# Kernel optimization log

Hardware: AMD Instinct MI355X
Metric: run time of the kernel (lower is better)

## Reference

```python
import jax, jax.numpy as jnp
import numpy as np

EMBED = 1024
HEADS = 16


def setup_inputs() -> dict:
    key = jax.random.key(0)
    k1, k2, k3 = jax.random.split(key, 3)
    B, S, D = 2, 2048, EMBED
    x = jax.random.normal(k1, (B, S, D), dtype=jnp.float32)
    # nn.Linear weights: stored as [out, in]; y = x @ W.T
    w_qkv = jax.random.normal(k2, (3 * D, D), dtype=jnp.float32) * (D ** -0.5)
    w_out = jax.random.normal(k3, (D, D), dtype=jnp.float32) * (D ** -0.5)
    return {"x": x, "w_qkv": w_qkv, "w_out": w_out}


def reference(x, w_qkv, w_out):
    B, S, D = x.shape
    H = HEADS
    hd = D // H
    qkv = x @ w_qkv.T                       # [B, S, 3D]
    q, k, v = jnp.split(qkv, 3, axis=-1)
    # 'b l (head k) -> b head l k'
    def heads(t):
        return t.reshape(B, S, H, hd).transpose(0, 2, 1, 3)
    q, k, v = heads(q), heads(k), heads(v)
    scale = hd ** 0.5
    scores = jnp.einsum('bhqd,bhkd->bhqk', q, k) / scale
    probs = jax.nn.softmax(scores, axis=-1)
    out = jnp.einsum('bhqk,bhkd->bhqd', probs, v)  # [B, H, S, hd]
    out = out.transpose(0, 2, 1, 3).reshape(B, S, D)
    return out @ w_out.T
```

## Files before the change

### kernel.cpp

```cpp
#include <hip/hip_runtime.h>

typedef short short8 __attribute__((ext_vector_type(8)));
typedef short short4v __attribute__((ext_vector_type(4)));
typedef float floatx4 __attribute__((ext_vector_type(4)));
typedef unsigned short ushort_t;

#define EMBED 1024
#define HEADS 16
#define HD 64
#define SEQ 2048
#define BATCH 2

__device__ inline ushort_t f2bf(float f) {
    unsigned int u = __float_as_uint(f);
    u += 0x7fff + ((u >> 16) & 1);
    return (ushort_t)(u >> 16);
}

typedef const __attribute__((address_space(1))) unsigned int* gas_t;
typedef __attribute__((address_space(3))) unsigned int* las_t;
__device__ inline void async_copy16(const ushort_t* g, ushort_t* l) {
    __builtin_amdgcn_global_load_lds((gas_t)g, (las_t)l, 16, 0, 0);
}

__global__ void cast3_kernel(const float* __restrict__ a, ushort_t* __restrict__ oa, int na,
                             const float* __restrict__ b, ushort_t* __restrict__ ob, int nb,
                             const float* __restrict__ c, ushort_t* __restrict__ oc, int nc) {
    int idx = (blockIdx.x * blockDim.x + threadIdx.x) * 4;
    const float* in; ushort_t* out;
    if (idx < na)            { in = a;  out = oa; }
    else if (idx < na + nb)  { in = b;  out = ob; idx -= na; }
    else if (idx < na + nb + nc) { in = c; out = oc; idx -= na + nb; }
    else return;
    float4 f = *(const float4*)(in + idx);
    ushort4 o;
    o.x = f2bf(f.x); o.y = f2bf(f.y); o.z = f2bf(f.z); o.w = f2bf(f.w);
    *(ushort4*)(out + idx) = o;
}

#define BM 128
#define BN 128
#define BK 64

template<int MODE>
__launch_bounds__(256, 3)
__global__ void gemm_bt(const ushort_t* __restrict__ A, const ushort_t* __restrict__ B,
                        float* __restrict__ outF,
                        ushort_t* __restrict__ qb, ushort_t* __restrict__ kb,
                        ushort_t* __restrict__ vtb,
                        int M, int N, int K) {
    __shared__ ushort_t As[BM * BK];
    __shared__ ushort_t Bs[BN * BK];
    const int id   = blockIdx.x;
    const int jj   = id >> 3;
    const int bm   = (id & 7) * 4 + (jj & 3);
    const int bn   = jj >> 2;
    const int t    = threadIdx.x;
    const int lane = t & 63;
    const int wave = t >> 6;
    const int wm   = (wave >> 1) * 64;
    const int wn   = (wave & 1) * 64;
    const int m0   = bm * BM;
    const int n0   = bn * BN;
    const int col  = lane & 15;
    const int quad = lane >> 4;

    const int srow = lane >> 3;
    const int sgr  = (lane & 7) ^ (srow & 7);
    const int slot0 = quad ^ (col & 7);

    floatx4 acc[4][4] = {};

    for (int k0 = 0; k0 < K; k0 += BK) {
        for (int half = 0; half < 4; ++half) {
            int row0 = wave * 32 + half * 8;
            int r = row0 + srow;
            async_copy16(A + (size_t)(m0 + r) * K + k0 + sgr * 8, &As[row0 * BK]);
            async_copy16(B + (size_t)(n0 + r) * K + k0 + sgr * 8, &Bs[row0 * BK]);
        }
        __syncthreads();
        short8 a[2][4], b[2][4];
        for (int i = 0; i < 4; ++i) {
            int base = (wm + i * 16 + col) * BK;
            a[0][i] = *(const short8*)(&As[base + slot0 * 8]);
            a[1][i] = *(const short8*)(&As[base + (slot0 ^ 4) * 8]);
        }
        for (int j = 0; j < 4; ++j) {
            int base = (wn + j * 16 + col) * BK;
            b[0][j] = *(const short8*)(&Bs[base + slot0 * 8]);
            b[1][j] = *(const short8*)(&Bs[base + (slot0 ^ 4) * 8]);
        }
        for (int kk = 0; kk < 2; ++kk)
            for (int i = 0; i < 4; ++i)
                for (int j = 0; j < 4; ++j)
                    acc[i][j] = __builtin_amdgcn_mfma_f32_16x16x32_bf16(a[kk][i], b[kk][j], acc[i][j], 0, 0, 0);
        __syncthreads();
    }

    for (int i = 0; i < 4; ++i)
        for (int j = 0; j < 4; ++j) {
            int n = n0 + wn + j * 16 + col;
            int mb = m0 + wm + i * 16 + quad * 4;
            if (MODE == 1) {
                for (int r = 0; r < 4; ++r)
                    outF[(size_t)(mb + r) * N + n] = acc[i][j][r];
            } else {
                int part = n >> 10;
                int within = n & 1023;
                int h = within >> 6, d = within & 63;
                int bb = mb >> 11, s = mb & 2047;
                if (part == 2) {
                    short4v pv;
                    pv.x = (short)f2bf(acc[i][j][0]); pv.y = (short)f2bf(acc[i][j][1]);
                    pv.z = (short)f2bf(acc[i][j][2]); pv.w = (short)f2bf(acc[i][j][3]);
                    *(short4v*)(vtb + (((size_t)bb * HEADS + h) * HD + d) * SEQ + s) = pv;
                } else {
                    ushort_t* dst = (part == 0) ? qb : kb;
                    for (int r = 0; r < 4; ++r)
                        dst[(((size_t)bb * HEADS + h) * SEQ + s + r) * HD + d] = f2bf(acc[i][j][r]);
                }
            }
        }
}

#define LDP 72

__launch_bounds__(256, 3)
__global__ void attn_kernel(const ushort_t* __restrict__ qb_, const ushort_t* __restrict__ kb,
                            const ushort_t* __restrict__ vtb, ushort_t* __restrict__ attn) {
    __shared__ ushort_t Klds[2][64 * 64];
    __shared__ ushort_t Vlds[2][64 * 64];
    __shared__ ushort_t Plds[4][2][16 * LDP];
    const int id   = blockIdx.x;
    const int jj   = id >> 3;
    const int bh   = (id & 7) * 4 + (jj >> 4);
    const int qblk = jj & 15;
    const int t    = threadIdx.x;
    const int lane = t & 63;
    const int wave = t >> 6;
    const int col  = lane & 15;
    const int quad = lane >> 4;
    const int q0   = qblk * 128 + wave * 32;

    const ushort_t* Q  = qb_ + (size_t)bh * SEQ * HD;
    const ushort_t* Kp = kb  + (size_t)bh * SEQ * HD;
    const ushort_t* Vt = vtb + (size_t)bh * HD * SEQ;

    const int srow = lane >> 3;
    const int sgr  = lane & 7;

    short8 qf[2][2];
    for (int qt = 0; qt < 2; ++qt) {
        qf[qt][0] = *(const short8*)(Q + (size_t)(q0 + qt * 16 + col) * HD + quad * 8);
        qf[qt][1] = *(const short8*)(Q + (size_t)(q0 + qt * 16 + col) * HD + 32 + quad * 8);
    }

    floatx4 acc[2][4] = {};
    float lsum[2] = {0.f, 0.f};
    const float SC = 0.125f * 1.44269504f;
    const int sw = col & 7;

    auto stage = [&](int kt, int buf) {
        for (int inst = 0; inst < 2; ++inst) {
            int row0 = wave * 16 + inst * 8;
            int r = row0 + srow;
            const ushort_t* gk = Kp + (size_t)(kt + r) * HD + ((sgr ^ (r & 7)) * 8);
            async_copy16(gk, &Klds[buf][row0 * 64]);
            const ushort_t* gv = Vt + (size_t)r * SEQ + kt + ((sgr ^ (r & 7)) * 8);
            async_copy16(gv, &Vlds[buf][row0 * 64]);
        }
    };

    stage(0, 0);
    __syncthreads();

    for (int kt = 0; kt < SEQ; kt += 64) {
        const int cur = (kt >> 6) & 1;
        stage((kt + 64) & (SEQ - 1), cur ^ 1);

        const ushort_t* Kc = Klds[cur];
        const ushort_t* Vc = Vlds[cur];

        short8 kf[4][2];
        for (int n = 0; n < 4; ++n) {
            int row = n * 16 + col;
            kf[n][0] = *(const short8*)(Kc + row * 64 + ((quad ^ sw) * 8));
            kf[n][1] = *(const short8*)(Kc + row * 64 + (((4 + quad) ^ sw) * 8));
        }
        for (int qt = 0; qt < 2; ++qt)
            for (int n = 0; n < 4; ++n) {
                floatx4 z = {};
                z = __builtin_amdgcn_mfma_f32_16x16x32_bf16(kf[n][0], qf[qt][0], z, 0, 0, 0);
                z = __builtin_amdgcn_mfma_f32_16x16x32_bf16(kf[n][1], qf[qt][1], z, 0, 0, 0);
                unsigned int u0 = __float_as_uint(__builtin_amdgcn_exp2f(z[0] * SC));
                unsigned int u1 = __float_as_uint(__builtin_amdgcn_exp2f(z[1] * SC));
                unsigned int u2 = __float_as_uint(__builtin_amdgcn_exp2f(z[2] * SC));
                unsigned int u3 = __float_as_uint(__builtin_amdgcn_exp2f(z[3] * SC));
                lsum[qt] += (__uint_as_float(u0 & 0xffff0000u) + __uint_as_float(u1 & 0xffff0000u))
                          + (__uint_as_float(u2 & 0xffff0000u) + __uint_as_float(u3 & 0xffff0000u));
                uint2 pk;
                pk.x = __builtin_amdgcn_perm(u1, u0, 0x07060302u);
                pk.y = __builtin_amdgcn_perm(u3, u2, 0x07060302u);
                *(uint2*)(&Plds[wave][qt][col * LDP + n * 16 + quad * 4]) = pk;
            }
        short8 vf[4][2];
        for (int d = 0; d < 4; ++d) {
            int row = d * 16 + col;
            vf[d][0] = *(const short8*)(Vc + row * 64 + ((quad ^ sw) * 8));
            vf[d][1] = *(const short8*)(Vc + row * 64 + (((4 + quad) ^ sw) * 8));
        }
        for (int qt = 0; qt < 2; ++qt) {
            short8 pf0 = *(const short8*)(&Plds[wave][qt][col * LDP + quad * 8]);
            short8 pf1 = *(const short8*)(&Plds[wave][qt][col * LDP + 32 + quad * 8]);
            for (int d = 0; d < 4; ++d) {
                acc[qt][d] = __builtin_amdgcn_mfma_f32_16x16x32_bf16(pf0, vf[d][0], acc[qt][d], 0, 0, 0);
                acc[qt][d] = __builtin_amdgcn_mfma_f32_16x16x32_bf16(pf1, vf[d][1], acc[qt][d], 0, 0, 0);
            }
        }
        __syncthreads();
    }

    int b = bh >> 4, h = bh & 15;
    for (int qt = 0; qt < 2; ++qt) {
        float s = lsum[qt];
        s += __shfl_xor(s, 16);
        s += __shfl_xor(s, 32);
        float inv[4];
        for (int r = 0; r < 4; ++r)
            inv[r] = 1.0f / __shfl(s, quad * 4 + r);
        for (int d = 0; d < 4; ++d)
            for (int r = 0; r < 4; ++r) {
                int row = q0 + qt * 16 + quad * 4 + r;
                int cc  = h * HD + d * 16 + col;
                attn[((size_t)b * SEQ + row) * EMBED + cc] = f2bf(acc[qt][d][r] * inv[r]);
            }
    }
}

extern "C" void kernel_launch(void* const* d_in, const int* in_sizes, int n_in,
                              void* d_out, int out_size, void* d_ws, size_t ws_size,
                              hipStream_t stream) {
    const float* x     = (const float*)d_in[0];
    const float* w_qkv = (const float*)d_in[1];
    const float* w_out = (const float*)d_in[2];
    float* out = (float*)d_out;

    char* ws = (char*)d_ws;
    size_t off = 0;
    ushort_t* x_bf    = (ushort_t*)(ws + off); off += (size_t)BATCH * SEQ * EMBED * 2;
    ushort_t* wqkv_bf = (ushort_t*)(ws + off); off += (size_t)3 * EMBED * EMBED * 2;
    ushort_t* wout_bf = (ushort_t*)(ws + off); off += (size_t)EMBED * EMBED * 2;
    ushort_t* q_buf   = (ushort_t*)(ws + off); off += (size_t)BATCH * HEADS * SEQ * HD * 2;
    ushort_t* k_buf   = (ushort_t*)(ws + off); off += (size_t)BATCH * HEADS * SEQ * HD * 2;
    ushort_t* vt_buf  = (ushort_t*)(ws + off); off += (size_t)BATCH * HEADS * SEQ * HD * 2;
    ushort_t* attn_bf = (ushort_t*)(ws + off); off += (size_t)BATCH * SEQ * EMBED * 2;

    int n_x = BATCH * SEQ * EMBED, n_wq = 3 * EMBED * EMBED, n_wo = EMBED * EMBED;
    int n_all = n_x + n_wq + n_wo;
    cast3_kernel<<<n_all / 1024, 256, 0, stream>>>(x, x_bf, n_x, w_qkv, wqkv_bf, n_wq,
                                                   w_out, wout_bf, n_wo);

    gemm_bt<0><<<768, 256, 0, stream>>>(
        x_bf, wqkv_bf, nullptr, q_buf, k_buf, vt_buf, BATCH * SEQ, 3 * EMBED, EMBED);

    attn_kernel<<<512, 256, 0, stream>>>(q_buf, k_buf, vt_buf, attn_bf);

    gemm_bt<1><<<256, 256, 0, stream>>>(
        attn_bf, wout_bf, out, nullptr, nullptr, nullptr, BATCH * SEQ, EMBED, EMBED);
}
```

Baseline: 179.6 us.

## Split attention KV loop across two wave groups and fold softmax scale into Q

The attention kernel now launches 512 threads per block. Two groups of four waves each process alternating 64-key chunks of the sequence, and their partial outputs and row sums are combined through LDS at the end. The softmax scale and log2(e) factor are folded into Q when the QKV GEMM writes it, which removes a multiply per score. The P tile is also processed in halves with a swizzled, smaller LDS buffer. The aim is more waves in flight to hide MFMA, exp and LDS latency, at the cost of an extra LDS reduction, more register pressure, and an extra rounding of the scaled Q to bf16.

```diff
diff --git a/kernel.cpp b/kernel.cpp
--- a/kernel.cpp
+++ b/kernel.cpp
@@ -10,6 +10,7 @@
 #define HD 64
 #define SEQ 2048
 #define BATCH 2
+#define QSCALE 0.18033688f
 
 __device__ inline ushort_t f2bf(float f) {
     unsigned int u = __float_as_uint(f);
@@ -116,21 +117,18 @@
                     *(short4v*)(vtb + (((size_t)bb * HEADS + h) * HD + d) * SEQ + s) = pv;
                 } else {
                     ushort_t* dst = (part == 0) ? qb : kb;
+                    const float scl = (part == 0) ? QSCALE : 1.0f;
                     for (int r = 0; r < 4; ++r)
-                        dst[(((size_t)bb * HEADS + h) * SEQ + s + r) * HD + d] = f2bf(acc[i][j][r]);
+                        dst[(((size_t)bb * HEADS + h) * SEQ + s + r) * HD + d] = f2bf(acc[i][j][r] * scl);
                 }
             }
         }
 }
 
-#define LDP 72
-
-__launch_bounds__(256, 3)
+__launch_bounds__(512, 4)
 __global__ void attn_kernel(const ushort_t* __restrict__ qb_, const ushort_t* __restrict__ kb,
                             const ushort_t* __restrict__ vtb, ushort_t* __restrict__ attn) {
-    __shared__ ushort_t Klds[2][64 * 64];
-    __shared__ ushort_t Vlds[2][64 * 64];
-    __shared__ ushort_t Plds[4][2][16 * LDP];
+    __shared__ __align__(16) ushort_t lds[36864];
     const int id   = blockIdx.x;
     const int jj   = id >> 3;
     const int bh   = (id & 7) * 4 + (jj >> 4);
@@ -138,18 +136,38 @@
     const int t    = threadIdx.x;
     const int lane = t & 63;
     const int wave = t >> 6;
+    const int g    = wave >> 2;
+    const int wv   = wave & 3;
     const int col  = lane & 15;
     const int quad = lane >> 4;
-    const int q0   = qblk * 128 + wave * 32;
+    const int q0   = qblk * 128 + wv * 32;
+    const int sw   = col & 7;
+    const int srow = lane >> 3;
+    const int sgr  = lane & 7;
 
     const ushort_t* Q  = qb_ + (size_t)bh * SEQ * HD;
     const ushort_t* Kp = kb  + (size_t)bh * SEQ * HD;
     const ushort_t* Vt = vtb + (size_t)bh * HD * SEQ;
 
-    const int srow = lane >> 3;
-    const int sgr  = lane & 7;
+    ushort_t* Kb0 = &lds[(g * 2) * 4096];
+    ushort_t* Vb0 = &lds[16384 + (g * 2) * 4096];
+    ushort_t* Pb  = &lds[32768 + wave * 512];
+
+    auto stage = [&](int c, int buf) {
+        int kt = c << 6;
+        #pragma unroll
+        for (int inst = 0; inst < 2; ++inst) {
+            int row0 = wv * 16 + inst * 8;
+            int r = row0 + srow;
+            async_copy16(Kp + (size_t)(kt + r) * HD + (sgr ^ (r & 7)) * 8,
+                         Kb0 + buf * 4096 + row0 * 64);
+            async_copy16(Vt + (size_t)r * SEQ + kt + (sgr ^ (r & 7)) * 8,
+                         Vb0 + buf * 4096 + row0 * 64);
+        }
+    };
 
     short8 qf[2][2];
+    #pragma unroll
     for (int qt = 0; qt < 2; ++qt) {
         qf[qt][0] = *(const short8*)(Q + (size_t)(q0 + qt * 16 + col) * HD + quad * 8);
         qf[qt][1] = *(const short8*)(Q + (size_t)(q0 + qt * 16 + col) * HD + 32 + quad * 8);
@@ -157,84 +175,93 @@
 
     floatx4 acc[2][4] = {};
     float lsum[2] = {0.f, 0.f};
-    const float SC = 0.125f * 1.44269504f;
-    const int sw = col & 7;
-
-    auto stage = [&](int kt, int buf) {
-        for (int inst = 0; inst < 2; ++inst) {
-            int row0 = wave * 16 + inst * 8;
-            int r = row0 + srow;
-            const ushort_t* gk = Kp + (size_t)(kt + r) * HD + ((sgr ^ (r & 7)) * 8);
-            async_copy16(gk, &Klds[buf][row0 * 64]);
-            const ushort_t* gv = Vt + (size_t)r * SEQ + kt + ((sgr ^ (r & 7)) * 8);
-            async_copy16(gv, &Vlds[buf][row0 * 64]);
-        }
-    };
-
-    stage(0, 0);
+
+    stage(g, 0);
     __syncthreads();
 
-    for (int kt = 0; kt < SEQ; kt += 64) {
-        const int cur = (kt >> 6) & 1;
-        stage((kt + 64) & (SEQ - 1), cur ^ 1);
-
-        const ushort_t* Kc = Klds[cur];
-        const ushort_t* Vc = Vlds[cur];
-
-        short8 kf[4][2];
-        for (int n = 0; n < 4; ++n) {
-            int row = n * 16 + col;
-            kf[n][0] = *(const short8*)(Kc + row * 64 + ((quad ^ sw) * 8));
-            kf[n][1] = *(const short8*)(Kc + row * 64 + (((4 + quad) ^ sw) * 8));
-        }
-        for (int qt = 0; qt < 2; ++qt)
-            for (int n = 0; n < 4; ++n) {
-                floatx4 z = {};
-                z = __builtin_amdgcn_mfma_f32_16x16x32_bf16(kf[n][0], qf[qt][0], z, 0, 0, 0);
-                z = __builtin_amdgcn_mfma_f32_16x16x32_bf16(kf[n][1], qf[qt][1], z, 0, 0, 0);
-                unsigned int u0 = __float_as_uint(__builtin_amdgcn_exp2f(z[0] * SC));
-                unsigned int u1 = __float_as_uint(__builtin_amdgcn_exp2f(z[1] * SC));
-                unsigned int u2 = __float_as_uint(__builtin_amdgcn_exp2f(z[2] * SC));
-                unsigned int u3 = __float_as_uint(__builtin_amdgcn_exp2f(z[3] * SC));
-                lsum[qt] += (__uint_as_float(u0 & 0xffff0000u) + __uint_as_float(u1 & 0xffff0000u))
-                          + (__uint_as_float(u2 & 0xffff0000u) + __uint_as_float(u3 & 0xffff0000u));
-                uint2 pk;
-                pk.x = __builtin_amdgcn_perm(u1, u0, 0x07060302u);
-                pk.y = __builtin_amdgcn_perm(u3, u2, 0x07060302u);
-                *(uint2*)(&Plds[wave][qt][col * LDP + n * 16 + quad * 4]) = pk;
-            }
-        short8 vf[4][2];
-        for (int d = 0; d < 4; ++d) {
-            int row = d * 16 + col;
-            vf[d][0] = *(const short8*)(Vc + row * 64 + ((quad ^ sw) * 8));
-            vf[d][1] = *(const short8*)(Vc + row * 64 + (((4 + quad) ^ sw) * 8));
-        }
-        for (int qt = 0; qt < 2; ++qt) {
-            short8 pf0 = *(const short8*)(&Plds[wave][qt][col * LDP + quad * 8]);
-            short8 pf1 = *(const short8*)(&Plds[wave][qt][col * LDP + 32 + quad * 8]);
+    for (int i = 0; i < 16; ++i) {
+        const int cur = i & 1;
+        if (i < 15) stage(2 * (i + 1) + g, cur ^ 1);
+        const ushort_t* Kc = Kb0 + cur * 4096;
+        const ushort_t* Vc = Vb0 + cur * 4096;
+
+        #pragma unroll
+        for (int h = 0; h < 2; ++h) {
+            short8 kf[2][2], vf[4];
+            #pragma unroll
+            for (int nl = 0; nl < 2; ++nl) {
+                int row = (2 * h + nl) * 16 + col;
+                kf[nl][0] = *(const short8*)(Kc + row * 64 + ((quad ^ sw) * 8));
+                kf[nl][1] = *(const short8*)(Kc + row * 64 + (((4 + quad) ^ sw) * 8));
+            }
+            #pragma unroll
             for (int d = 0; d < 4; ++d) {
-                acc[qt][d] = __builtin_amdgcn_mfma_f32_16x16x32_bf16(pf0, vf[d][0], acc[qt][d], 0, 0, 0);
-                acc[qt][d] = __builtin_amdgcn_mfma_f32_16x16x32_bf16(pf1, vf[d][1], acc[qt][d], 0, 0, 0);
+                int row = d * 16 + col;
+                vf[d] = *(const short8*)(Vc + row * 64 + (((4 * h + quad) ^ sw) * 8));
+            }
+            #pragma unroll
+            for (int qt = 0; qt < 2; ++qt) {
+                #pragma unroll
+                for (int nl = 0; nl < 2; ++nl) {
+                    floatx4 z = {};
+                    z = __builtin_amdgcn_mfma_f32_16x16x32_bf16(kf[nl][0], qf[qt][0], z, 0, 0, 0);
+                    z = __builtin_amdgcn_mfma_f32_16x16x32_bf16(kf[nl][1], qf[qt][1], z, 0, 0, 0);
+                    unsigned u0 = __float_as_uint(__builtin_amdgcn_exp2f(z[0]));
+                    unsigned u1 = __float_as_uint(__builtin_amdgcn_exp2f(z[1]));
+                    unsigned u2 = __float_as_uint(__builtin_amdgcn_exp2f(z[2]));
+                    unsigned u3 = __float_as_uint(__builtin_amdgcn_exp2f(z[3]));
+                    lsum[qt] += (__uint_as_float(u0 & 0xffff0000u) + __uint_as_float(u1 & 0xffff0000u))
+                              + (__uint_as_float(u2 & 0xffff0000u) + __uint_as_float(u3 & 0xffff0000u));
+                    uint2 pk;
+                    pk.x = __builtin_amdgcn_perm(u1, u0, 0x07060302u);
+                    pk.y = __builtin_amdgcn_perm(u3, u2, 0x07060302u);
+                    int gl = nl * 2 + (quad >> 1);
+                    *(uint2*)(&Pb[col * 32 + ((gl ^ (col & 3)) << 3) + ((quad & 1) << 2)]) = pk;
+                }
+                short8 pf = *(const short8*)(&Pb[col * 32 + ((quad ^ (col & 3)) << 3)]);
+                #pragma unroll
+                for (int d = 0; d < 4; ++d)
+                    acc[qt][d] = __builtin_amdgcn_mfma_f32_16x16x32_bf16(pf, vf[d], acc[qt][d], 0, 0, 0);
             }
         }
         __syncthreads();
     }
 
-    int b = bh >> 4, h = bh & 15;
-    for (int qt = 0; qt < 2; ++qt) {
-        float s = lsum[qt];
-        s += __shfl_xor(s, 16);
-        s += __shfl_xor(s, 32);
-        float inv[4];
-        for (int r = 0; r < 4; ++r)
-            inv[r] = 1.0f / __shfl(s, quad * 4 + r);
-        for (int d = 0; d < 4; ++d)
-            for (int r = 0; r < 4; ++r) {
-                int row = q0 + qt * 16 + quad * 4 + r;
-                int cc  = h * HD + d * 16 + col;
-                attn[((size_t)b * SEQ + row) * EMBED + cc] = f2bf(acc[qt][d][r] * inv[r]);
-            }
-    }
+    float* fs = (float*)lds;
+    const int slot = (wave * 64 + lane) * 20;
+    floatx4 accK[4];
+    float lsK;
+    if (g == 0) {
+        #pragma unroll
+        for (int d = 0; d < 4; ++d) { *(floatx4*)(&fs[slot + d * 4]) = acc[1][d]; accK[d] = acc[0][d]; }
+        fs[slot + 16] = lsum[1]; lsK = lsum[0];
+    } else {
+        #pragma unroll
+        for (int d = 0; d < 4; ++d) { *(floatx4*)(&fs[slot + d * 4]) = acc[0][d]; accK[d] = acc[1][d]; }
+        fs[slot + 16] = lsum[0]; lsK = lsum[1];
+    }
+    __syncthreads();
+    const int pslot = ((wave ^ 4) * 64 + lane) * 20;
+    #pragma unroll
+    for (int d = 0; d < 4; ++d)
+        accK[d] += *(const floatx4*)(&fs[pslot + d * 4]);
+    float s = lsK + fs[pslot + 16];
+    s += __shfl_xor(s, 16);
+    s += __shfl_xor(s, 32);
+    float inv[4];
+    #pragma unroll
+    for (int r = 0; r < 4; ++r)
+        inv[r] = 1.0f / __shfl(s, quad * 4 + r);
+
+    int b = bh >> 4, hh = bh & 15;
+    #pragma unroll
+    for (int d = 0; d < 4; ++d)
+        #pragma unroll
+        for (int r = 0; r < 4; ++r) {
+            int row = q0 + g * 16 + quad * 4 + r;
+            int cc  = hh * HD + d * 16 + col;
+            attn[((size_t)b * SEQ + row) * EMBED + cc] = f2bf(accK[d][r] * inv[r]);
+        }
 }
 
 extern "C" void kernel_launch(void* const* d_in, const int* in_sizes, int n_in,
@@ -263,7 +290,7 @@
     gemm_bt<0><<<768, 256, 0, stream>>>(
         x_bf, wqkv_bf, nullptr, q_buf, k_buf, vt_buf, BATCH * SEQ, 3 * EMBED, EMBED);
 
-    attn_kernel<<<512, 256, 0, stream>>>(q_buf, k_buf, vt_buf, attn_bf);
+    attn_kernel<<<512, 512, 0, stream>>>(q_buf, k_buf, vt_buf, attn_bf);
 
     gemm_bt<1><<<256, 256, 0, stream>>>(
         attn_bf, wout_bf, out, nullptr, nullptr, nullptr, BATCH * SEQ, EMBED, EMBED);
```

Measured after the change: 178.8 us. No clear change (-0.5%).
